# Performance work log

Hardware: AMD Instinct MI355X
Metric: run time of the kernel (lower is better)

Reference implementation:

```python
import jax, jax.numpy as jnp
import numpy as np

N = 50000      # num vertices
E = 600000     # num incidence pairs
M = 100000     # num hyperedges
IN = 256       # in_channels
H = 8          # heads
C = 32         # out_channels per head


def setup_inputs() -> dict:
    key = jax.random.key(0)
    k = jax.random.split(key, 5)
    X = jax.random.normal(k[0], (N, IN), jnp.float32)
    W = jax.random.normal(k[1], (IN, H * C), jnp.float32) * (1.0 / np.sqrt(IN))
    att_e = jax.random.normal(k[2], (1, H, C), jnp.float32) * 0.1
    vertex = jax.random.randint(k[3], (E,), 0, N)
    edges = jax.random.randint(k[4], (E,), 0, M)
    return {"X": X, "W": W, "att_e": att_e, "vertex": vertex, "edges": edges, "num_edges": M}


def reference(X, W, att_e, vertex, edges, num_edges):
    n, h, c = X.shape[0], att_e.shape[1], att_e.shape[2]
    X0 = X @ W                              # [N, H*C]
    Xh = X0.reshape(n, h, c)                # [N, H, C]
    Xve = Xh[vertex]                        # [E, H, C] gather node feats per incidence
    # mean-aggregate incidences -> hyperedge features
    cnt = jax.ops.segment_sum(jnp.ones((vertex.shape[0],), X.dtype), edges, num_segments=num_edges)
    Xe = jax.ops.segment_sum(Xve, edges, num_segments=num_edges) / jnp.maximum(cnt, 1.0)[:, None, None]  # [M, H, C]
    alpha_e = jnp.sum(Xe * att_e, axis=-1)  # [M, H]
    a_ev = alpha_e[edges]                   # [E, H]
    alpha = jnp.where(a_ev >= 0, a_ev, 0.2 * a_ev)  # leaky_relu(0.2)
    # numerically stable segment softmax over incidences grouped by vertex
    amax = jax.ops.segment_max(alpha, vertex, num_segments=n)[vertex]
    aexp = jnp.exp(alpha - amax)
    asum = jax.ops.segment_sum(aexp, vertex, num_segments=n)[vertex]
    attn = aexp / (asum + 1e-16)            # [E, H]
    Xev = Xe[edges] * attn[:, :, None]      # [E, H, C]
    Xv = jax.ops.segment_sum(Xev, vertex, num_segments=n)  # [N, H, C]
    return jax.nn.gelu(Xv.reshape(n, h * c), approximate=False)
```

## Files before the change

### kernel.cpp

```cpp
#include <hip/hip_runtime.h>
#include <hip/hip_bf16.h>
#include <math.h>

#define NV 50000
#define NE 600000
#define NM 100000
#define KIN 256
#define HCC 256
#define NHH 8

#define SCAN_NB0 25
#define SCAN_NB1 13

#define CNT_B 2344
#define GEMM_BX 782
#define GEMM_B (GEMM_BX * 4)

typedef unsigned int u32;
typedef unsigned short u16;
typedef _Float16 f16;
typedef _Float16 v8h __attribute__((ext_vector_type(8)));
typedef _Float16 v4h __attribute__((ext_vector_type(4)));
typedef float v4f __attribute__((ext_vector_type(4)));

__global__ __launch_bounds__(256) void k_count_gemm(const int* __restrict__ vertex,
                                                    const int* __restrict__ edges,
                                                    int* __restrict__ e_hist,
                                                    int* __restrict__ v_hist,
                                                    u16* __restrict__ r_e,
                                                    u16* __restrict__ r_v,
                                                    const float* __restrict__ X,
                                                    const float* __restrict__ W,
                                                    f16* __restrict__ X0) {
    __shared__ __align__(16) f16 sA[64][72];
    __shared__ __align__(16) f16 sB[64][72];
    const int bid = blockIdx.x;
    const int t = threadIdx.x;
    if (bid < CNT_B) {
        int i = bid * 256 + t;
        if (i < NE) {
            int v = vertex[i], m = edges[i];
            r_e[i] = (u16)atomicAdd(e_hist + m + 1, 1);
            r_v[i] = (u16)atomicAdd(v_hist + v + 1, 1);
        }
        return;
    }
    const int g = bid - CNT_B;
    const int r0 = (g >> 2) * 64;
    const int c0 = (g & 3) * 64;
    const int wave = t >> 6;
    const int lane = t & 63;
    const int quad = lane >> 4;
    const int l16 = lane & 15;
    const int wr = wave & 1;
    const int wc = wave >> 1;

    v4f acc[2][2] = {{{0.f,0.f,0.f,0.f},{0.f,0.f,0.f,0.f}},
                     {{0.f,0.f,0.f,0.f},{0.f,0.f,0.f,0.f}}};

    for (int kc = 0; kc < KIN; kc += 64) {
        __syncthreads();
        #pragma unroll
        for (int i = 0; i < 4; ++i) {
            int lin = i * 256 + t;
            int row = lin >> 4;
            int k = (lin & 15) * 4;
            int gr = r0 + row;
            float4 x = make_float4(0.f, 0.f, 0.f, 0.f);
            if (gr < NV) x = *(const float4*)(X + (size_t)gr * KIN + kc + k);
            v4h hv = { (f16)x.x, (f16)x.y, (f16)x.z, (f16)x.w };
            *(v4h*)&sA[row][k] = hv;
        }
        #pragma unroll
        for (int i = 0; i < 4; ++i) {
            int lin = i * 256 + t;
            int k = lin >> 4;
            int n = (lin & 15) * 4;
            float4 b = *(const float4*)(W + (size_t)(kc + k) * HCC + c0 + n);
            sB[n + 0][k] = (f16)b.x;
            sB[n + 1][k] = (f16)b.y;
            sB[n + 2][k] = (f16)b.z;
            sB[n + 3][k] = (f16)b.w;
        }
        __syncthreads();
        #pragma unroll
        for (int ks = 0; ks < 2; ++ks) {
            const int kb = ks * 32 + quad * 8;
            v8h a[2], b[2];
            #pragma unroll
            for (int rf = 0; rf < 2; ++rf)
                a[rf] = *(const v8h*)&sA[wr * 32 + rf * 16 + l16][kb];
            #pragma unroll
            for (int cf = 0; cf < 2; ++cf)
                b[cf] = *(const v8h*)&sB[wc * 32 + cf * 16 + l16][kb];
            #pragma unroll
            for (int rf = 0; rf < 2; ++rf)
                #pragma unroll
                for (int cf = 0; cf < 2; ++cf)
                    acc[rf][cf] = __builtin_amdgcn_mfma_f32_16x16x32_f16(a[rf], b[cf], acc[rf][cf], 0, 0, 0);
        }
    }
    #pragma unroll
    for (int rf = 0; rf < 2; ++rf)
        #pragma unroll
        for (int cf = 0; cf < 2; ++cf)
            #pragma unroll
            for (int r = 0; r < 4; ++r) {
                int grow = r0 + wr * 32 + rf * 16 + quad * 4 + r;
                if (grow < NV)
                    X0[(size_t)grow * HCC + c0 + wc * 32 + cf * 16 + l16] = (f16)acc[rf][cf][r];
            }
}

__global__ __launch_bounds__(1024) void k_scan_blk(int* __restrict__ a0,
                                                   int* __restrict__ a1,
                                                   int* __restrict__ bsum) {
    const int b = blockIdx.x;
    int* a;
    int n, base;
    if (b < SCAN_NB0) { a = a0; n = NM + 1; base = b * 4096; }
    else              { a = a1; n = NV + 1; base = (b - SCAN_NB0) * 4096; }
    const int t = threadIdx.x;
    const int lane = t & 63, w = t >> 6;
    const int i = base + t * 4;
    int4 v = make_int4(0, 0, 0, 0);
    if (i + 3 < n) v = *(const int4*)(a + i);
    else if (i < n) {
        v.x = a[i];
        if (i + 1 < n) v.y = a[i + 1];
        if (i + 2 < n) v.z = a[i + 2];
    }
    v.y += v.x; v.z += v.y; v.w += v.z;
    int s = v.w;
    #pragma unroll
    for (int d = 1; d < 64; d <<= 1) {
        int x = __shfl_up(s, d, 64);
        if (lane >= d) s += x;
    }
    __shared__ int partials[16];
    __shared__ int woff[16];
    if (lane == 63) partials[w] = s;
    __syncthreads();
    if (t < 16) {
        int p = partials[t];
        int ps = p;
        #pragma unroll
        for (int d = 1; d < 16; d <<= 1) {
            int x = __shfl_up(ps, d, 64);
            if (t >= d) ps += x;
        }
        woff[t] = ps - p;
        if (t == 15) bsum[b] = ps;
    }
    __syncthreads();
    const int add = (s - v.w) + woff[w];
    v.x += add; v.y += add; v.z += add; v.w += add;
    if (i + 3 < n) *(int4*)(a + i) = v;
    else if (i < n) {
        a[i] = v.x;
        if (i + 1 < n) a[i + 1] = v.y;
        if (i + 2 < n) a[i + 2] = v.z;
    }
}

__global__ __launch_bounds__(1024) void k_scan_add(int* __restrict__ a0,
                                                   int* __restrict__ a1,
                                                   const int* __restrict__ bsum) {
    const int b = blockIdx.x;
    int* a;
    int n, bs0, blocal;
    if (b < SCAN_NB0) { a = a0; n = NM + 1; bs0 = 0;        blocal = b; }
    else              { a = a1; n = NV + 1; bs0 = SCAN_NB0; blocal = b - SCAN_NB0; }
    const int t = threadIdx.x;
    const int lane = t & 63;
    int x = (lane < blocal) ? bsum[bs0 + lane] : 0;
    #pragma unroll
    for (int d = 1; d < 64; d <<= 1) x += __shfl_xor(x, d, 64);
    const int off = x;
    if (off == 0 && blocal == 0) {  }
    const int i = blocal * 4096 + t * 4;
    if (i + 3 < n) {
        int4 v = *(const int4*)(a + i);
        v.x += off; v.y += off; v.z += off; v.w += off;
        *(int4*)(a + i) = v;
    } else if (i < n) {
        a[i] += off;
        if (i + 1 < n) a[i + 1] += off;
        if (i + 2 < n) a[i + 2] += off;
    }
}

__global__ __launch_bounds__(256) void k_efill(const int* __restrict__ vertex,
                                               const int* __restrict__ edges,
                                               const u16* __restrict__ r_e,
                                               const int* __restrict__ e_start,
                                               int* __restrict__ e_list) {
    int i = blockIdx.x * 256 + threadIdx.x;
    if (i >= NE) return;
    int m = edges[i];
    e_list[e_start[m] + (int)r_e[i]] = vertex[i];
}

__global__ __launch_bounds__(256) void k_vfill_egather(const int* __restrict__ vertex,
                                                       const int* __restrict__ edges,
                                                       const u16* __restrict__ r_v,
                                                       const int* __restrict__ v_start,
                                                       int* __restrict__ v_list,
                                                       const int* __restrict__ e_start,
                                                       const int* __restrict__ e_list,
                                                       const f16* __restrict__ X0,
                                                       const float* __restrict__ att,
                                                       f16* __restrict__ Xe,
                                                       float* __restrict__ alpha_e) {
    const int bid = blockIdx.x;
    if (bid < CNT_B) {
        int i = bid * 256 + threadIdx.x;
        if (i < NE) {
            int v = vertex[i];
            v_list[v_start[v] + (int)r_v[i]] = edges[i];
        }
        return;
    }
    int m = (bid - CNT_B) * 4 + (threadIdx.x >> 6);
    int lane = threadIdx.x & 63;
    int s0 = e_start[m], s1 = e_start[m + 1];
    int c = lane * 4;
    float4 acc = make_float4(0.f, 0.f, 0.f, 0.f);
    int i = s0;
    for (; i + 3 < s1; i += 4) {
        int v0 = e_list[i], v1 = e_list[i + 1], v2 = e_list[i + 2], v3 = e_list[i + 3];
        v4h x0 = *(const v4h*)(X0 + (size_t)v0 * HCC + c);
        v4h x1 = *(const v4h*)(X0 + (size_t)v1 * HCC + c);
        v4h x2 = *(const v4h*)(X0 + (size_t)v2 * HCC + c);
        v4h x3 = *(const v4h*)(X0 + (size_t)v3 * HCC + c);
        acc.x += (float)x0[0] + (float)x1[0] + (float)x2[0] + (float)x3[0];
        acc.y += (float)x0[1] + (float)x1[1] + (float)x2[1] + (float)x3[1];
        acc.z += (float)x0[2] + (float)x1[2] + (float)x2[2] + (float)x3[2];
        acc.w += (float)x0[3] + (float)x1[3] + (float)x2[3] + (float)x3[3];
    }
    for (; i < s1; ++i) {
        int v0 = e_list[i];
        v4h x0 = *(const v4h*)(X0 + (size_t)v0 * HCC + c);
        acc.x += (float)x0[0];
        acc.y += (float)x0[1];
        acc.z += (float)x0[2];
        acc.w += (float)x0[3];
    }
    float inv = 1.0f / fmaxf((float)(s1 - s0), 1.0f);
    acc.x *= inv; acc.y *= inv; acc.z *= inv; acc.w *= inv;
    v4h xev = { (f16)acc.x, (f16)acc.y, (f16)acc.z, (f16)acc.w };
    *(v4h*)(Xe + (size_t)m * HCC + c) = xev;
    float4 av = *(const float4*)(att + c);
    float p = acc.x * av.x + acc.y * av.y + acc.z * av.z + acc.w * av.w;
    p += __shfl_xor(p, 1, 64);
    p += __shfl_xor(p, 2, 64);
    p += __shfl_xor(p, 4, 64);
    if ((lane & 7) == 0) alpha_e[m * NHH + (lane >> 3)] = p;
}

__global__ __launch_bounds__(256) void k_vertex_gather(const int* __restrict__ v_start,
                                                       const int* __restrict__ v_list,
                                                       const f16* __restrict__ Xe,
                                                       const float* __restrict__ alpha_e,
                                                       float* __restrict__ out) {
    int v = blockIdx.x * 4 + (threadIdx.x >> 6);
    int lane = threadIdx.x & 63;
    int s0 = v_start[v], s1 = v_start[v + 1];
    int h = lane >> 3;
    int c = lane * 4;
    float4 acc = make_float4(0.f, 0.f, 0.f, 0.f);
    float se = 0.f;
    int i = s0;
    for (; i + 1 < s1; i += 2) {
        int m0 = v_list[i], m1 = v_list[i + 1];
        float a0 = alpha_e[m0 * NHH + h];
        float a1 = alpha_e[m1 * NHH + h];
        v4h x0 = *(const v4h*)(Xe + (size_t)m0 * HCC + c);
        v4h x1 = *(const v4h*)(Xe + (size_t)m1 * HCC + c);
        a0 = (a0 >= 0.f) ? a0 : 0.2f * a0;
        a1 = (a1 >= 0.f) ? a1 : 0.2f * a1;
        float e0 = __expf(a0);
        float e1 = __expf(a1);
        acc.x += e0 * (float)x0[0] + e1 * (float)x1[0];
        acc.y += e0 * (float)x0[1] + e1 * (float)x1[1];
        acc.z += e0 * (float)x0[2] + e1 * (float)x1[2];
        acc.w += e0 * (float)x0[3] + e1 * (float)x1[3];
        se += e0 + e1;
    }
    if (i < s1) {
        int m0 = v_list[i];
        float a0 = alpha_e[m0 * NHH + h];
        v4h x0 = *(const v4h*)(Xe + (size_t)m0 * HCC + c);
        a0 = (a0 >= 0.f) ? a0 : 0.2f * a0;
        float e0 = __expf(a0);
        acc.x += e0 * (float)x0[0];
        acc.y += e0 * (float)x0[1];
        acc.z += e0 * (float)x0[2];
        acc.w += e0 * (float)x0[3];
        se += e0;
    }
    float inv = 1.0f / (se + 1e-16f);
    float4 o;
    float xx;
    xx = acc.x * inv; o.x = 0.5f * xx * (1.f + erff(xx * 0.70710678118f));
    xx = acc.y * inv; o.y = 0.5f * xx * (1.f + erff(xx * 0.70710678118f));
    xx = acc.z * inv; o.z = 0.5f * xx * (1.f + erff(xx * 0.70710678118f));
    xx = acc.w * inv; o.w = 0.5f * xx * (1.f + erff(xx * 0.70710678118f));
    *(float4*)(out + (size_t)v * HCC + c) = o;
}

extern "C" void kernel_launch(void* const* d_in, const int* in_sizes, int n_in,
                              void* d_out, int out_size, void* d_ws, size_t ws_size,
                              hipStream_t stream) {
    const float* X = (const float*)d_in[0];
    const float* W = (const float*)d_in[1];
    const float* att = (const float*)d_in[2];
    const int* vertex = (const int*)d_in[3];
    const int* edges = (const int*)d_in[4];
    float* out = (float*)d_out;

    char* ws = (char*)d_ws;
    size_t off = 0;
    #define WS_TAKE(bytes) (ws + off); off += (((size_t)(bytes)) + 15) & ~(size_t)15
    f16* X0 = (f16*)WS_TAKE((size_t)NV * HCC * 2);
    f16* Xe = (f16*)WS_TAKE((size_t)NM * HCC * 2);
    float* alpha_e = (float*)WS_TAKE((size_t)NM * NHH * 4);
    int* e_start = (int*)WS_TAKE((size_t)(NM + 1) * 4);
    int* v_start = (int*)WS_TAKE((size_t)(NV + 1) * 4);
    int* e_list = (int*)WS_TAKE((size_t)NE * 4);
    int* v_list = (int*)WS_TAKE((size_t)NE * 4);
    u16* r_e = (u16*)WS_TAKE((size_t)NE * 2);
    u16* r_v = (u16*)WS_TAKE((size_t)NE * 2);
    int* bsum = (int*)WS_TAKE(64 * 4);
    #undef WS_TAKE

    size_t hist_bytes = (((size_t)(NM + 1) * 4 + 15) & ~(size_t)15) +
                        (((size_t)(NV + 1) * 4 + 15) & ~(size_t)15);
    hipMemsetAsync(e_start, 0, hist_bytes, stream);

    k_count_gemm<<<CNT_B + GEMM_B, 256, 0, stream>>>(vertex, edges, e_start, v_start,
                                                     r_e, r_v, X, W, X0);
    k_scan_blk<<<SCAN_NB0 + SCAN_NB1, 1024, 0, stream>>>(e_start, v_start, bsum);
    k_scan_add<<<SCAN_NB0 + SCAN_NB1, 1024, 0, stream>>>(e_start, v_start, bsum);
    k_efill<<<CNT_B, 256, 0, stream>>>(vertex, edges, r_e, e_start, e_list);
    k_vfill_egather<<<CNT_B + NM / 4, 256, 0, stream>>>(vertex, edges, r_v, v_start, v_list,
                                                        e_start, e_list, X0, att, Xe, alpha_e);
    k_vertex_gather<<<NV / 4, 256, 0, stream>>>(v_start, v_list, Xe, alpha_e, out);
}
```

Measured before the change: 318.8 us.

## Privatize incidence histograms into 8 partitions and swizzle GEMM block order

The counting atomics now go into 8 private copies of the edge and vertex histograms, chosen by block index, to cut atomic contention. A new merge kernel turns the per-partition counts into per-partition offsets and writes the totals for the existing scan. The fill kernels add the partition offset when placing entries in the CSR lists. The GEMM blocks are also remapped so groups of 8 row tiles share column tiles, for better cache reuse. The cost is a larger memset, an extra kernel launch and extra reads of the partition arrays.

```diff
diff --git a/kernel.cpp b/kernel.cpp
--- a/kernel.cpp
+++ b/kernel.cpp
@@ -8,13 +8,17 @@
 #define KIN 256
 #define HCC 256
 #define NHH 8
+#define NP 8
 
 #define SCAN_NB0 25
 #define SCAN_NB1 13
 
+#define MRG_B0 98
+#define MRG_B1 49
+
 #define CNT_B 2344
-#define GEMM_BX 782
-#define GEMM_B (GEMM_BX * 4)
+#define GEMM_RG 784
+#define GEMM_B (GEMM_RG * 4)
 
 typedef unsigned int u32;
 typedef unsigned short u16;
@@ -25,8 +29,8 @@
 
 __global__ __launch_bounds__(256) void k_count_gemm(const int* __restrict__ vertex,
                                                     const int* __restrict__ edges,
-                                                    int* __restrict__ e_hist,
-                                                    int* __restrict__ v_hist,
+                                                    int* __restrict__ eh8,
+                                                    int* __restrict__ vh8,
                                                     u16* __restrict__ r_e,
                                                     u16* __restrict__ r_v,
                                                     const float* __restrict__ X,
@@ -40,14 +44,20 @@
         int i = bid * 256 + t;
         if (i < NE) {
             int v = vertex[i], m = edges[i];
-            r_e[i] = (u16)atomicAdd(e_hist + m + 1, 1);
-            r_v[i] = (u16)atomicAdd(v_hist + v + 1, 1);
+            int p = bid & (NP - 1);
+            int* ehp = eh8 + (size_t)p * (NM + 1);
+            int* vhp = vh8 + (size_t)p * (NV + 1);
+            r_e[i] = (u16)atomicAdd(ehp + m + 1, 1);
+            r_v[i] = (u16)atomicAdd(vhp + v + 1, 1);
         }
         return;
     }
     const int g = bid - CNT_B;
-    const int r0 = (g >> 2) * 64;
-    const int c0 = (g & 3) * 64;
+    const int rg = (g >> 5) * 8 + (g & 7);
+    const int cg = (g >> 3) & 3;
+    if (rg >= (NV + 63) / 64) return;
+    const int r0 = rg * 64;
+    const int c0 = cg * 64;
     const int wave = t >> 6;
     const int lane = t & 63;
     const int quad = lane >> 4;
@@ -110,6 +120,29 @@
                 if (grow < NV)
                     X0[(size_t)grow * HCC + c0 + wc * 32 + cf * 16 + l16] = (f16)acc[rf][cf][r];
             }
+}
+
+__global__ __launch_bounds__(1024) void k_merge(int* __restrict__ eh8,
+                                                int* __restrict__ vh8,
+                                                int* __restrict__ e_start,
+                                                int* __restrict__ v_start) {
+    const int b = blockIdx.x;
+    int* h8;
+    int* outp;
+    int nk, stride, k;
+    if (b < MRG_B0) { h8 = eh8; outp = e_start; nk = NM; stride = NM + 1; k = b * 1024 + threadIdx.x; }
+    else            { h8 = vh8; outp = v_start; nk = NV; stride = NV + 1; k = (b - MRG_B0) * 1024 + threadIdx.x; }
+    if (k >= nk) return;
+    int* hp = h8 + k + 1;
+    int s = 0;
+    #pragma unroll
+    for (int p = 0; p < NP; ++p) {
+        int t = *hp;
+        *hp = s;
+        s += t;
+        hp += stride;
+    }
+    outp[k + 1] = s;
 }
 
 __global__ __launch_bounds__(1024) void k_scan_blk(int* __restrict__ a0,
@@ -177,7 +210,6 @@
     #pragma unroll
     for (int d = 1; d < 64; d <<= 1) x += __shfl_xor(x, d, 64);
     const int off = x;
-    if (off == 0 && blocal == 0) {  }
     const int i = blocal * 4096 + t * 4;
     if (i + 3 < n) {
         int4 v = *(const int4*)(a + i);
@@ -194,17 +226,21 @@
                                                const int* __restrict__ edges,
                                                const u16* __restrict__ r_e,
                                                const int* __restrict__ e_start,
+                                               const int* __restrict__ eh8,
                                                int* __restrict__ e_list) {
     int i = blockIdx.x * 256 + threadIdx.x;
     if (i >= NE) return;
     int m = edges[i];
-    e_list[e_start[m] + (int)r_e[i]] = vertex[i];
+    int p = (i >> 8) & (NP - 1);
+    int pos = e_start[m] + eh8[(size_t)p * (NM + 1) + m + 1] + (int)r_e[i];
+    e_list[pos] = vertex[i];
 }
 
 __global__ __launch_bounds__(256) void k_vfill_egather(const int* __restrict__ vertex,
                                                        const int* __restrict__ edges,
                                                        const u16* __restrict__ r_v,
                                                        const int* __restrict__ v_start,
+                                                       const int* __restrict__ vh8,
                                                        int* __restrict__ v_list,
                                                        const int* __restrict__ e_start,
                                                        const int* __restrict__ e_list,
@@ -217,7 +253,9 @@
         int i = bid * 256 + threadIdx.x;
         if (i < NE) {
             int v = vertex[i];
-            v_list[v_start[v] + (int)r_v[i]] = edges[i];
+            int p = (i >> 8) & (NP - 1);
+            int pos = v_start[v] + vh8[(size_t)p * (NV + 1) + v + 1] + (int)r_v[i];
+            v_list[pos] = edges[i];
         }
         return;
     }
@@ -325,8 +363,12 @@
     f16* X0 = (f16*)WS_TAKE((size_t)NV * HCC * 2);
     f16* Xe = (f16*)WS_TAKE((size_t)NM * HCC * 2);
     float* alpha_e = (float*)WS_TAKE((size_t)NM * NHH * 4);
+    size_t z0 = off;
     int* e_start = (int*)WS_TAKE((size_t)(NM + 1) * 4);
     int* v_start = (int*)WS_TAKE((size_t)(NV + 1) * 4);
+    int* eh8 = (int*)WS_TAKE((size_t)NP * (NM + 1) * 4);
+    int* vh8 = (int*)WS_TAKE((size_t)NP * (NV + 1) * 4);
+    size_t z1 = off;
     int* e_list = (int*)WS_TAKE((size_t)NE * 4);
     int* v_list = (int*)WS_TAKE((size_t)NE * 4);
     u16* r_e = (u16*)WS_TAKE((size_t)NE * 2);
@@ -334,16 +376,15 @@
     int* bsum = (int*)WS_TAKE(64 * 4);
     #undef WS_TAKE
 
-    size_t hist_bytes = (((size_t)(NM + 1) * 4 + 15) & ~(size_t)15) +
-                        (((size_t)(NV + 1) * 4 + 15) & ~(size_t)15);
-    hipMemsetAsync(e_start, 0, hist_bytes, stream);
-
-    k_count_gemm<<<CNT_B + GEMM_B, 256, 0, stream>>>(vertex, edges, e_start, v_start,
+    hipMemsetAsync(e_start, 0, z1 - z0, stream);
+
+    k_count_gemm<<<CNT_B + GEMM_B, 256, 0, stream>>>(vertex, edges, eh8, vh8,
                                                      r_e, r_v, X, W, X0);
+    k_merge<<<MRG_B0 + MRG_B1, 1024, 0, stream>>>(eh8, vh8, e_start, v_start);
     k_scan_blk<<<SCAN_NB0 + SCAN_NB1, 1024, 0, stream>>>(e_start, v_start, bsum);
     k_scan_add<<<SCAN_NB0 + SCAN_NB1, 1024, 0, stream>>>(e_start, v_start, bsum);
-    k_efill<<<CNT_B, 256, 0, stream>>>(vertex, edges, r_e, e_start, e_list);
-    k_vfill_egather<<<CNT_B + NM / 4, 256, 0, stream>>>(vertex, edges, r_v, v_start, v_list,
+    k_efill<<<CNT_B, 256, 0, stream>>>(vertex, edges, r_e, e_start, eh8, e_list);
+    k_vfill_egather<<<CNT_B + NM / 4, 256, 0, stream>>>(vertex, edges, r_v, v_start, vh8, v_list,
                                                         e_start, e_list, X0, att, Xe, alpha_e);
     k_vertex_gather<<<NV / 4, 256, 0, stream>>>(v_start, v_list, Xe, alpha_e, out);
 }
```

New measurement: 326.7 us. 2.5% more time.

## Replace global atomic counting with chunked LDS histograms and column scan

Applied to the files above, without the earlier changes.

The global-atomic counting pass for edge and vertex degrees is replaced by per-chunk shared-memory histograms with packed 16-bit counters over key ranges, followed by a column-wise prefix over the chunks. The fill kernels then add a per-chunk offset when computing list positions. The GEMM becomes a separate kernel with a swizzled block-to-tile mapping intended to improve cache locality. The aim is to remove heavily contended global atomics, at the cost of extra launches, extra chunk-count traffic, and serializing the GEMM after the counting work it previously overlapped with.

```diff
diff --git a/kernel.cpp b/kernel.cpp
--- a/kernel.cpp
+++ b/kernel.cpp
@@ -9,12 +9,18 @@
 #define HCC 256
 #define NHH 8
 
+#define NCH 32
+#define CHUNK 18750
+#define KRANGE 25000
+#define HIST_B (NCH * 6)
+#define CSCAN_B 74
+
 #define SCAN_NB0 25
 #define SCAN_NB1 13
 
 #define CNT_B 2344
-#define GEMM_BX 782
-#define GEMM_B (GEMM_BX * 4)
+#define GEMM_RG 784
+#define GEMM_B (GEMM_RG * 4)
 
 typedef unsigned int u32;
 typedef unsigned short u16;
@@ -23,31 +29,77 @@
 typedef _Float16 v4h __attribute__((ext_vector_type(4)));
 typedef float v4f __attribute__((ext_vector_type(4)));
 
-__global__ __launch_bounds__(256) void k_count_gemm(const int* __restrict__ vertex,
-                                                    const int* __restrict__ edges,
-                                                    int* __restrict__ e_hist,
-                                                    int* __restrict__ v_hist,
-                                                    u16* __restrict__ r_e,
-                                                    u16* __restrict__ r_v,
-                                                    const float* __restrict__ X,
-                                                    const float* __restrict__ W,
-                                                    f16* __restrict__ X0) {
+__global__ __launch_bounds__(256) void k_hist(const int* __restrict__ vertex,
+                                              const int* __restrict__ edges,
+                                              u16* __restrict__ r_e,
+                                              u16* __restrict__ r_v,
+                                              u16* __restrict__ Ce,
+                                              u16* __restrict__ Cv) {
+    __shared__ __align__(16) u32 hist[KRANGE / 2];
+    const int bid = blockIdx.x;
+    const int t = threadIdx.x;
+    const int pass = bid >> 5;
+    const int chunk = bid & (NCH - 1);
+    const bool eside = pass < 4;
+    const int kbase = (eside ? pass : pass - 4) * KRANGE;
+    const int* keys = eside ? edges : vertex;
+    u16* rout = eside ? r_e : r_v;
+    u16* crow = eside ? (Ce + (size_t)chunk * NM) : (Cv + (size_t)chunk * NV);
+
+    uint4* h4 = (uint4*)hist;
+    for (int j = t; j < KRANGE / 8; j += 256) h4[j] = make_uint4(0u, 0u, 0u, 0u);
+    __syncthreads();
+
+    const int i0 = chunk * CHUNK;
+    for (int i = i0 + t; i < i0 + CHUNK; i += 256) {
+        int k = keys[i] - kbase;
+        if ((u32)k < (u32)KRANGE) {
+            int sh = (k & 1) << 4;
+            u32 old = atomicAdd(&hist[k >> 1], 1u << sh);
+            rout[i] = (u16)(old >> sh);
+        }
+    }
+    __syncthreads();
+
+    uint4* d4 = (uint4*)(crow + kbase);
+    for (int j = t; j < KRANGE / 8; j += 256) d4[j] = h4[j];
+}
+
+__global__ __launch_bounds__(1024) void k_cscan(u16* __restrict__ Ce,
+                                                u16* __restrict__ Cv,
+                                                int* __restrict__ e_start,
+                                                int* __restrict__ v_start) {
+    int tid = blockIdx.x * 1024 + threadIdx.x;
+    u32* mat;
+    int* outp;
+    int col, ncol;
+    if (tid < NM / 2)               { mat = (u32*)Ce; outp = e_start; col = tid;          ncol = NM / 2; }
+    else if (tid < NM / 2 + NV / 2) { mat = (u32*)Cv; outp = v_start; col = tid - NM / 2; ncol = NV / 2; }
+    else return;
+    u32 s = 0;
+    u32* p = mat + col;
+    for (int c = 0; c < NCH; ++c) {
+        u32 o = *p;
+        *p = s;
+        s += o;
+        p += ncol;
+    }
+    outp[2 * col + 1] = (int)(s & 0xffffu);
+    outp[2 * col + 2] = (int)(s >> 16);
+}
+
+__global__ __launch_bounds__(256) void k_gemm(const float* __restrict__ X,
+                                              const float* __restrict__ W,
+                                              f16* __restrict__ X0) {
     __shared__ __align__(16) f16 sA[64][72];
     __shared__ __align__(16) f16 sB[64][72];
-    const int bid = blockIdx.x;
+    const int g = blockIdx.x;
+    const int rg = (g >> 5) * 8 + (g & 7);
+    const int cg = (g >> 3) & 3;
+    if (rg >= (NV + 63) / 64) return;
     const int t = threadIdx.x;
-    if (bid < CNT_B) {
-        int i = bid * 256 + t;
-        if (i < NE) {
-            int v = vertex[i], m = edges[i];
-            r_e[i] = (u16)atomicAdd(e_hist + m + 1, 1);
-            r_v[i] = (u16)atomicAdd(v_hist + v + 1, 1);
-        }
-        return;
-    }
-    const int g = bid - CNT_B;
-    const int r0 = (g >> 2) * 64;
-    const int c0 = (g & 3) * 64;
+    const int r0 = rg * 64;
+    const int c0 = cg * 64;
     const int wave = t >> 6;
     const int lane = t & 63;
     const int quad = lane >> 4;
@@ -177,7 +229,6 @@
     #pragma unroll
     for (int d = 1; d < 64; d <<= 1) x += __shfl_xor(x, d, 64);
     const int off = x;
-    if (off == 0 && blocal == 0) {  }
     const int i = blocal * 4096 + t * 4;
     if (i + 3 < n) {
         int4 v = *(const int4*)(a + i);
@@ -194,17 +245,21 @@
                                                const int* __restrict__ edges,
                                                const u16* __restrict__ r_e,
                                                const int* __restrict__ e_start,
+                                               const u16* __restrict__ Ce,
                                                int* __restrict__ e_list) {
     int i = blockIdx.x * 256 + threadIdx.x;
     if (i >= NE) return;
     int m = edges[i];
-    e_list[e_start[m] + (int)r_e[i]] = vertex[i];
+    int chunk = i / CHUNK;
+    int pos = e_start[m] + (int)Ce[(size_t)chunk * NM + m] + (int)r_e[i];
+    e_list[pos] = vertex[i];
 }
 
 __global__ __launch_bounds__(256) void k_vfill_egather(const int* __restrict__ vertex,
                                                        const int* __restrict__ edges,
                                                        const u16* __restrict__ r_v,
                                                        const int* __restrict__ v_start,
+                                                       const u16* __restrict__ Cv,
                                                        int* __restrict__ v_list,
                                                        const int* __restrict__ e_start,
                                                        const int* __restrict__ e_list,
@@ -217,7 +272,9 @@
         int i = bid * 256 + threadIdx.x;
         if (i < NE) {
             int v = vertex[i];
-            v_list[v_start[v] + (int)r_v[i]] = edges[i];
+            int chunk = i / CHUNK;
+            int pos = v_start[v] + (int)Cv[(size_t)chunk * NV + v] + (int)r_v[i];
+            v_list[pos] = edges[i];
         }
         return;
     }
@@ -325,25 +382,28 @@
     f16* X0 = (f16*)WS_TAKE((size_t)NV * HCC * 2);
     f16* Xe = (f16*)WS_TAKE((size_t)NM * HCC * 2);
     float* alpha_e = (float*)WS_TAKE((size_t)NM * NHH * 4);
+    size_t z0 = off;
     int* e_start = (int*)WS_TAKE((size_t)(NM + 1) * 4);
     int* v_start = (int*)WS_TAKE((size_t)(NV + 1) * 4);
+    size_t z1 = off;
     int* e_list = (int*)WS_TAKE((size_t)NE * 4);
     int* v_list = (int*)WS_TAKE((size_t)NE * 4);
     u16* r_e = (u16*)WS_TAKE((size_t)NE * 2);
     u16* r_v = (u16*)WS_TAKE((size_t)NE * 2);
+    u16* Ce = (u16*)WS_TAKE((size_t)NCH * NM * 2);
+    u16* Cv = (u16*)WS_TAKE((size_t)NCH * NV * 2);
     int* bsum = (int*)WS_TAKE(64 * 4);
     #undef WS_TAKE
 
-    size_t hist_bytes = (((size_t)(NM + 1) * 4 + 15) & ~(size_t)15) +
-                        (((size_t)(NV + 1) * 4 + 15) & ~(size_t)15);
-    hipMemsetAsync(e_start, 0, hist_bytes, stream);
-
-    k_count_gemm<<<CNT_B + GEMM_B, 256, 0, stream>>>(vertex, edges, e_start, v_start,
-                                                     r_e, r_v, X, W, X0);
+    hipMemsetAsync(e_start, 0, z1 - z0, stream);
+
+    k_hist<<<HIST_B, 256, 0, stream>>>(vertex, edges, r_e, r_v, Ce, Cv);
+    k_cscan<<<CSCAN_B, 1024, 0, stream>>>(Ce, Cv, e_start, v_start);
     k_scan_blk<<<SCAN_NB0 + SCAN_NB1, 1024, 0, stream>>>(e_start, v_start, bsum);
     k_scan_add<<<SCAN_NB0 + SCAN_NB1, 1024, 0, stream>>>(e_start, v_start, bsum);
-    k_efill<<<CNT_B, 256, 0, stream>>>(vertex, edges, r_e, e_start, e_list);
-    k_vfill_egather<<<CNT_B + NM / 4, 256, 0, stream>>>(vertex, edges, r_v, v_start, v_list,
+    k_gemm<<<GEMM_B, 256, 0, stream>>>(X, W, X0);
+    k_efill<<<CNT_B, 256, 0, stream>>>(vertex, edges, r_e, e_start, Ce, e_list);
+    k_vfill_egather<<<CNT_B + NM / 4, 256, 0, stream>>>(vertex, edges, r_v, v_start, Cv, v_list,
                                                         e_start, e_list, X0, att, Xe, alpha_e);
     k_vertex_gather<<<NV / 4, 256, 0, stream>>>(v_start, v_list, Xe, alpha_e, out);
 }
```

Result: slower. 328.0 us (+2.9%).
